# Performance work log

Hardware: AMD Instinct MI355X
Metric: run time of the kernel (lower is better)

## Reference

```python
import jax, jax.numpy as jnp
import numpy as np

B, S, D, H, E, K = 4, 2048, 1024, 512, 64, 8


def setup_inputs() -> dict:
    key = jax.random.key(0)
    k1, k2, k3, k4 = jax.random.split(key, 4)
    x = jax.random.normal(k1, (B, S, D), dtype=jnp.float32)
    # gate weight stored as [D, E] (equivalent to torch Linear weight [E, D] transposed)
    Wg = jax.random.normal(k2, (D, E), dtype=jnp.float32) * (1.0 / np.sqrt(D))
    Wup = jax.random.normal(k3, (E, D, H), dtype=jnp.float32) * (1.0 / np.sqrt(D))
    Wdown = jax.random.normal(k4, (E, H, D), dtype=jnp.float32) * (1.0 / np.sqrt(H))
    return {"x": x, "Wg": Wg, "Wup": Wup, "Wdown": Wdown}


def reference(x, Wg, Wup, Wdown):
    # NOTE: ExpertMLP.forward in the source ignores gate_proj: out = down(silu(up(x)))
    T = B * S
    flat = x.reshape(T, D)                        # [T, D]
    logits = flat @ Wg                            # [T, E]
    topk_scores, topk_idx = jax.lax.top_k(logits, K)   # [T, K]
    gate_w = jax.nn.softmax(topk_scores, axis=-1)       # [T, K]
    # dense combine matrix [T, E]; topk indices are unique per token
    rows = jnp.arange(T)[:, None]
    combine = jnp.zeros((T, E), dtype=x.dtype).at[rows, topk_idx].set(gate_w)
    # scan over experts: each expert runs on all tokens, masked/weighted by combine
    def body(acc, params):
        wu, wd, c = params                         # [D,H], [H,D], [T]
        h = jax.nn.silu(flat @ wu)                 # [T, H]
        y = h @ wd                                 # [T, D]
        return acc + c[:, None] * y, None
    out0 = jnp.zeros((T, D), dtype=x.dtype)
    out, _ = jax.lax.scan(body, out0, (Wup, Wdown, combine.T))
    return out.reshape(B, S, D)
```

## Files before the change

kernel.cpp:

```cpp
#include <hip/hip_runtime.h>
#include <hip/hip_bf16.h>
#include <stdint.h>
#include <math.h>

#define T_TOK 8192
#define DDIM  1024
#define HDIM  512
#define NEXP  64
#define TOPK  8
#define CHUNKS 16

typedef __bf16 bf16x8 __attribute__((ext_vector_type(8)));
typedef float  f32x4  __attribute__((ext_vector_type(4)));

__device__ __forceinline__ void load_lds16(const void* gp, void* lp){
  __builtin_amdgcn_global_load_lds(
      (__attribute__((address_space(1))) void*)(uintptr_t)gp,
      (__attribute__((address_space(3))) void*)lp, 16, 0, 0);
}

__device__ __forceinline__ unsigned short f2bfbits(float f){
  union { __bf16 b; unsigned short u; } cv; cv.b = (__bf16)f; return cv.u;
}
__device__ __forceinline__ float bf2f(unsigned short s){
  unsigned int u = ((unsigned int)s) << 16; return __uint_as_float(u);
}

__global__ __launch_bounds__(256) void k_cvt_x(const float* __restrict__ x,
                                               __bf16* __restrict__ xb){
  size_t i   = (size_t)blockIdx.x * 256 + threadIdx.x;
  size_t off = i * 8;
  float4 v0 = *(const float4*)(x + off);
  float4 v1 = *(const float4*)(x + off + 4);
  bf16x8 o;
  o[0]=(__bf16)v0.x; o[1]=(__bf16)v0.y; o[2]=(__bf16)v0.z; o[3]=(__bf16)v0.w;
  o[4]=(__bf16)v1.x; o[5]=(__bf16)v1.y; o[6]=(__bf16)v1.z; o[7]=(__bf16)v1.w;
  *(bf16x8*)(xb + off) = o;
}

__global__ __launch_bounds__(256) void k_transpose_cvt(const float* __restrict__ src,
                                                       __bf16* __restrict__ dst,
                                                       int R, int C){
  __shared__ float tile[32][33];
  int z  = blockIdx.z;
  int c0 = blockIdx.x * 32;
  int r0 = blockIdx.y * 32;
  const float* s = src + (size_t)z * R * C;
  __bf16*      d = dst + (size_t)z * R * C;
  int tx = threadIdx.x, ty = threadIdx.y;
  #pragma unroll
  for (int i = ty; i < 32; i += 8)
    tile[i][tx] = s[(size_t)(r0 + i) * C + c0 + tx];
  __syncthreads();
  #pragma unroll
  for (int i = ty; i < 32; i += 8)
    d[(size_t)(c0 + i) * R + r0 + tx] = (__bf16)tile[tx][i];
}

__global__ __launch_bounds__(256) void k_gate(const float* __restrict__ x,
                                              const float* __restrict__ Wg,
                                              float* __restrict__ logits){
  __shared__ float xs[32][64];
  __shared__ float ws[32][64];
  const int tid = threadIdx.x;
  const int m0  = blockIdx.x * 64;
  const int tm  = (tid >> 4) << 2;
  const int tn  = (tid & 15) << 2;
  const int sr  = tid >> 2;
  const int sc  = tid & 3;
  double acc[4][4];
  #pragma unroll
  for (int i=0;i<4;i++)
    #pragma unroll
    for (int j=0;j<4;j++) acc[i][j]=0.0;

  for (int k0 = 0; k0 < DDIM; k0 += 32){
    {
      const float4* g = (const float4*)(Wg + (size_t)k0 * 64);
      float4* l = (float4*)&ws[0][0];
      l[tid]       = g[tid];
      l[tid + 256] = g[tid + 256];
    }
    {
      const float* g = x + (size_t)(m0 + sr) * DDIM + k0 + sc * 8;
      float4 a = *(const float4*)g;
      float4 b = *(const float4*)(g + 4);
      xs[sc*8+0][sr]=a.x; xs[sc*8+1][sr]=a.y; xs[sc*8+2][sr]=a.z; xs[sc*8+3][sr]=a.w;
      xs[sc*8+4][sr]=b.x; xs[sc*8+5][sr]=b.y; xs[sc*8+6][sr]=b.z; xs[sc*8+7][sr]=b.w;
    }
    __syncthreads();
    for (int k = 0; k < 32; k++){
      float4 a4 = *(const float4*)&xs[k][tm];
      float4 b4 = *(const float4*)&ws[k][tn];
      float av[4] = {a4.x,a4.y,a4.z,a4.w};
      float bv[4] = {b4.x,b4.y,b4.z,b4.w};
      #pragma unroll
      for (int i=0;i<4;i++)
        #pragma unroll
        for (int j=0;j<4;j++)
          acc[i][j] += (double)av[i] * (double)bv[j];
    }
    __syncthreads();
  }
  #pragma unroll
  for (int i=0;i<4;i++){
    float4 o = make_float4((float)acc[i][0],(float)acc[i][1],(float)acc[i][2],(float)acc[i][3]);
    *(float4*)&logits[(size_t)(m0 + tm + i) * 64 + tn] = o;
  }
}

__global__ __launch_bounds__(256) void k_topk(const float* __restrict__ logits,
                                              int* __restrict__ tk_idx,
                                              float* __restrict__ tk_w){
  const int lane = threadIdx.x & 63;
  const int t    = blockIdx.x * 4 + (threadIdx.x >> 6);
  float v = logits[(size_t)t * 64 + lane];
  const int myi = lane;
  float mv[8]; int mi[8];
  #pragma unroll
  for (int k = 0; k < 8; k++){
    float bv = v; int bi = myi;
    #pragma unroll
    for (int off = 32; off > 0; off >>= 1){
      float ov = __shfl_xor(bv, off, 64);
      int   oi = __shfl_xor(bi, off, 64);
      if (ov > bv || (ov == bv && oi < bi)){ bv = ov; bi = oi; }
    }
    mv[k] = bv; mi[k] = bi;
    if (bi == myi) v = -INFINITY;
  }
  float w[8]; float s = 0.f;
  #pragma unroll
  for (int k = 0; k < 8; k++){ w[k] = expf(mv[k] - mv[0]); s += w[k]; }
  float inv = 1.0f / s;
  if (lane == 0){
    #pragma unroll
    for (int k = 0; k < 8; k++){
      tk_idx[(size_t)t * 8 + k] = mi[k];
      tk_w [(size_t)t * 8 + k] = w[k] * inv;
    }
  }
}

__global__ __launch_bounds__(256) void k_hist(const int* __restrict__ tk_idx,
                                              int* __restrict__ g_hist){
  __shared__ int h[4][64];
  const int tid = threadIdx.x, wave = tid >> 6;
  ((int*)h)[tid] = 0;
  __syncthreads();
  const int4* p = (const int4*)(tk_idx + blockIdx.x * 4096);
  #pragma unroll
  for (int i = 0; i < 4; i++){
    int4 v = p[i * 256 + tid];
    atomicAdd(&h[wave][v.x], 1); atomicAdd(&h[wave][v.y], 1);
    atomicAdd(&h[wave][v.z], 1); atomicAdd(&h[wave][v.w], 1);
  }
  __syncthreads();
  if (tid < 64)
    g_hist[blockIdx.x * 64 + tid] = h[0][tid] + h[1][tid] + h[2][tid] + h[3][tid];
}

__global__ void k_scan(const int* __restrict__ g_hist,
                       int* __restrict__ offsets,
                       int* __restrict__ g_base){
  const int e = threadIdx.x;
  int h[CHUNKS]; int tot = 0;
  #pragma unroll
  for (int c = 0; c < CHUNKS; c++){ h[c] = g_hist[c * 64 + e]; tot += h[c]; }
  int inc = tot;
  #pragma unroll
  for (int off = 1; off < 64; off <<= 1){
    int n = __shfl_up(inc, off, 64);
    if (e >= off) inc += n;
  }
  int exc = inc - tot;
  offsets[e] = exc;
  if (e == 63) offsets[64] = inc;
  int b = exc;
  #pragma unroll
  for (int c = 0; c < CHUNKS; c++){ g_base[c * 64 + e] = b; b += h[c]; }
}

__global__ __launch_bounds__(256) void k_scatter(const int* __restrict__ tk_idx,
                                                 const int* __restrict__ g_base,
                                                 int* __restrict__ slot_token,
                                                 int* __restrict__ inv_pos){
  __shared__ int cnt[64];
  const int tid = threadIdx.x;
  if (tid < 64) cnt[tid] = g_base[blockIdx.x * 64 + tid];
  __syncthreads();
  const int base = blockIdx.x * 4096;
  #pragma unroll
  for (int i = 0; i < 16; i++){
    int gid = base + i * 256 + tid;
    int e = tk_idx[gid];
    int pos = atomicAdd(&cnt[e], 1);
    slot_token[pos] = gid >> 3;
    inv_pos[gid] = pos;
  }
}

__global__ __launch_bounds__(256) void k_gemm1(const __bf16* __restrict__ xb,
                                               const __bf16* __restrict__ wupT,
                                               const int* __restrict__ offsets,
                                               const int* __restrict__ slot_token,
                                               __bf16* __restrict__ h){
  const int e    = blockIdx.z;
  const int base = offsets[e];
  const int ne   = offsets[e + 1] - base;
  const int m0   = blockIdx.x * 128;
  if (m0 >= ne) return;
  const int n0   = blockIdx.y * 128;

  __shared__ __align__(16) __bf16 As[128 * 32];
  __shared__ __align__(16) __bf16 Bs[128 * 32];
  __shared__ int s_tok[128];

  const int tid = threadIdx.x;
  if (tid < 128){
    int r = m0 + tid;
    s_tok[tid] = slot_token[base + (r < ne ? r : 0)];
  }
  __syncthreads();

  const int wave = tid >> 6, lane = tid & 63;
  const int wm = (wave >> 1) << 6, wn = (wave & 1) << 6;
  const int sr = lane >> 2, sc = lane & 3;
  const int fr = lane & 15, fk = (lane >> 4) << 3;
  const __bf16* wB = wupT + (size_t)e * HDIM * DDIM + (size_t)n0 * DDIM;

  f32x4 zero = {0.f, 0.f, 0.f, 0.f};
  f32x4 acc[4][4];
  #pragma unroll
  for (int i=0;i<4;i++)
    #pragma unroll
    for (int j=0;j<4;j++) acc[i][j] = zero;

  for (int k0 = 0; k0 < DDIM; k0 += 32){
    #pragma unroll
    for (int q = 0; q < 2; q++){
      int rr = (wave << 5) + (q << 4) + sr;
      const __bf16* g = xb + (size_t)s_tok[rr] * DDIM + k0 + (sc << 3);
      load_lds16(g, (void*)&As[((wave << 1) + q) << 9]);
    }
    #pragma unroll
    for (int q = 0; q < 2; q++){
      int rr = (wave << 5) + (q << 4) + sr;
      const __bf16* g = wB + (size_t)rr * DDIM + k0 + (sc << 3);
      load_lds16(g, (void*)&Bs[((wave << 1) + q) << 9]);
    }
    __syncthreads();
    bf16x8 af[4], bg[4];
    #pragma unroll
    for (int i=0;i<4;i++) af[i] = *(const bf16x8*)&As[((wm + (i<<4) + fr) << 5) + fk];
    #pragma unroll
    for (int j=0;j<4;j++) bg[j] = *(const bf16x8*)&Bs[((wn + (j<<4) + fr) << 5) + fk];
    #pragma unroll
    for (int i=0;i<4;i++)
      #pragma unroll
      for (int j=0;j<4;j++)
        acc[i][j] = __builtin_amdgcn_mfma_f32_16x16x32_bf16(af[i], bg[j], acc[i][j], 0, 0, 0);
    __syncthreads();
  }

  const int cr = (lane >> 4) << 2, cc = lane & 15;
  #pragma unroll
  for (int i=0;i<4;i++){
    #pragma unroll
    for (int reg=0;reg<4;reg++){
      int rl = wm + (i << 4) + cr + reg;
      int gm = m0 + rl;
      if (gm < ne){
        __bf16* hrow = h + (size_t)(base + gm) * HDIM + n0 + wn;
        #pragma unroll
        for (int j=0;j<4;j++){
          float v  = acc[i][j][reg];
          float sv = v / (1.0f + __expf(-v));
          unsigned short u = f2bfbits(sv);
          int part = __shfl_xor((int)u, 1, 64);
          if (!(lane & 1)){
            unsigned int packed = ((unsigned int)(unsigned short)part << 16) | u;
            *(unsigned int*)((unsigned short*)hrow + (j << 4) + cc) = packed;
          }
        }
      }
    }
  }
}

__global__ __launch_bounds__(256) void k_gemm2(const __bf16* __restrict__ h,
                                               const __bf16* __restrict__ wdownT,
                                               const int* __restrict__ offsets,
                                               __bf16* __restrict__ y,
                                               int elo){
  const int e    = elo + blockIdx.z;
  const int base = offsets[e];
  const int ne   = offsets[e + 1] - base;
  const int m0   = blockIdx.x * 128;
  if (m0 >= ne) return;
  const int n0   = blockIdx.y * 128;
  const int ybase = offsets[elo];

  __shared__ __align__(16) __bf16 As[128 * 32];
  __shared__ __align__(16) __bf16 Bs[128 * 32];

  const int tid = threadIdx.x;
  const int wave = tid >> 6, lane = tid & 63;
  const int wm = (wave >> 1) << 6, wn = (wave & 1) << 6;
  const int sr = lane >> 2, sc = lane & 3;
  const int fr = lane & 15, fk = (lane >> 4) << 3;
  const __bf16* wB = wdownT + (size_t)e * DDIM * HDIM + (size_t)n0 * HDIM;

  f32x4 zero = {0.f, 0.f, 0.f, 0.f};
  f32x4 acc[4][4];
  #pragma unroll
  for (int i=0;i<4;i++)
    #pragma unroll
    for (int j=0;j<4;j++) acc[i][j] = zero;

  for (int k0 = 0; k0 < HDIM; k0 += 32){
    #pragma unroll
    for (int q = 0; q < 2; q++){
      int rr = (wave << 5) + (q << 4) + sr;
      int sl = (m0 + rr < ne) ? (m0 + rr) : 0;
      const __bf16* g = h + (size_t)(base + sl) * HDIM + k0 + (sc << 3);
      load_lds16(g, (void*)&As[((wave << 1) + q) << 9]);
    }
    #pragma unroll
    for (int q = 0; q < 2; q++){
      int rr = (wave << 5) + (q << 4) + sr;
      const __bf16* g = wB + (size_t)rr * HDIM + k0 + (sc << 3);
      load_lds16(g, (void*)&Bs[((wave << 1) + q) << 9]);
    }
    __syncthreads();
    bf16x8 af[4], bg[4];
    #pragma unroll
    for (int i=0;i<4;i++) af[i] = *(const bf16x8*)&As[((wm + (i<<4) + fr) << 5) + fk];
    #pragma unroll
    for (int j=0;j<4;j++) bg[j] = *(const bf16x8*)&Bs[((wn + (j<<4) + fr) << 5) + fk];
    #pragma unroll
    for (int i=0;i<4;i++)
      #pragma unroll
      for (int j=0;j<4;j++)
        acc[i][j] = __builtin_amdgcn_mfma_f32_16x16x32_bf16(af[i], bg[j], acc[i][j], 0, 0, 0);
    __syncthreads();
  }

  const int cr = (lane >> 4) << 2, cc = lane & 15;
  #pragma unroll
  for (int i=0;i<4;i++){
    #pragma unroll
    for (int reg=0;reg<4;reg++){
      int rl = wm + (i << 4) + cr + reg;
      int gm = m0 + rl;
      if (gm < ne){
        __bf16* yrow = y + (size_t)(base - ybase + gm) * DDIM + n0 + wn;
        #pragma unroll
        for (int j=0;j<4;j++){
          unsigned short u = f2bfbits(acc[i][j][reg]);
          int part = __shfl_xor((int)u, 1, 64);
          if (!(lane & 1)){
            unsigned int packed = ((unsigned int)(unsigned short)part << 16) | u;
            *(unsigned int*)((unsigned short*)yrow + (j << 4) + cc) = packed;
          }
        }
      }
    }
  }
}

__global__ __launch_bounds__(256) void k_combine(const __bf16* __restrict__ y,
                                                 const int* __restrict__ tk_idx,
                                                 const float* __restrict__ tk_w,
                                                 const int* __restrict__ inv_pos,
                                                 const int* __restrict__ offsets,
                                                 float* __restrict__ out,
                                                 int elo, int ehi, int first){
  const int t   = blockIdx.x;
  const int tid = threadIdx.x;
  __shared__ int se[8]; __shared__ float sw[8]; __shared__ int sp[8];
  if (tid < 8){
    se[tid] = tk_idx[(size_t)t * 8 + tid];
    sw[tid] = tk_w [(size_t)t * 8 + tid];
    sp[tid] = inv_pos[(size_t)t * 8 + tid];
  }
  __syncthreads();
  const int ybase = offsets[elo];
  const int c = tid << 2;
  float4 acc;
  if (first) acc = make_float4(0.f, 0.f, 0.f, 0.f);
  else       acc = *(const float4*)&out[(size_t)t * DDIM + c];
  #pragma unroll
  for (int k = 0; k < 8; k++){
    int e = se[k];
    if (e >= elo && e < ehi){
      const unsigned short* yr = (const unsigned short*)y + (size_t)(sp[k] - ybase) * DDIM + c;
      ushort4 raw = *(const ushort4*)yr;
      float w = sw[k];
      acc.x += w * bf2f(raw.x);
      acc.y += w * bf2f(raw.y);
      acc.z += w * bf2f(raw.z);
      acc.w += w * bf2f(raw.w);
    }
  }
  *(float4*)&out[(size_t)t * DDIM + c] = acc;
}

extern "C" void kernel_launch(void* const* d_in, const int* in_sizes, int n_in,
                              void* d_out, int out_size, void* d_ws, size_t ws_size,
                              hipStream_t stream){
  const float* x     = (const float*)d_in[0];
  const float* Wg    = (const float*)d_in[1];
  const float* Wup   = (const float*)d_in[2];
  const float* Wdown = (const float*)d_in[3];
  float* out = (float*)d_out;

  char* ws = (char*)d_ws;
  size_t off = 0;
  auto alloc = [&](size_t bytes) -> void* {
    void* p = ws + off;
    off += (bytes + 255) & ~(size_t)255;
    return p;
  };
  __bf16* wupT      = (__bf16*)alloc((size_t)NEXP * DDIM * HDIM * 2);
  __bf16* xb        = (__bf16*)alloc((size_t)T_TOK * DDIM * 2);
  float*  logits    = (float*)alloc((size_t)T_TOK * NEXP * 4);
  __bf16* wdownT    = (__bf16*)alloc((size_t)NEXP * DDIM * HDIM * 2);
  __bf16* hbuf      = (__bf16*)alloc((size_t)T_TOK * TOPK * HDIM * 2);
  int*    tk_idx    = (int*)  alloc((size_t)T_TOK * TOPK * 4);
  float*  tk_w      = (float*)alloc((size_t)T_TOK * TOPK * 4);
  int*    slot_tok  = (int*)  alloc((size_t)T_TOK * TOPK * 4);
  int*    inv_pos   = (int*)  alloc((size_t)T_TOK * TOPK * 4);
  int*    g_hist    = (int*)  alloc((size_t)CHUNKS * 64 * 4);
  int*    g_base    = (int*)  alloc((size_t)CHUNKS * 64 * 4);
  int*    offsets   = (int*)  alloc(512);
  __bf16* ybuf      = (__bf16*)ws;

  k_cvt_x<<<4096, 256, 0, stream>>>(x, xb);
  k_transpose_cvt<<<dim3(16, 32, 64), dim3(32, 8), 0, stream>>>(Wup,   wupT,   DDIM, HDIM);
  k_transpose_cvt<<<dim3(32, 16, 64), dim3(32, 8), 0, stream>>>(Wdown, wdownT, HDIM, DDIM);
  k_gate<<<T_TOK / 64, 256, 0, stream>>>(x, Wg, logits);
  k_topk<<<T_TOK / 4, 256, 0, stream>>>(logits, tk_idx, tk_w);
  k_hist<<<CHUNKS, 256, 0, stream>>>(tk_idx, g_hist);
  k_scan<<<1, 64, 0, stream>>>(g_hist, offsets, g_base);
  k_scatter<<<CHUNKS, 256, 0, stream>>>(tk_idx, g_base, slot_tok, inv_pos);
  k_gemm1<<<dim3(16, 4, 64), 256, 0, stream>>>(xb, wupT, offsets, slot_tok, hbuf);
  k_gemm2<<<dim3(16, 8, 32), 256, 0, stream>>>(hbuf, wdownT, offsets, ybuf, 0);
  k_combine<<<T_TOK, 256, 0, stream>>>(ybuf, tk_idx, tk_w, inv_pos, offsets, out, 0, 32, 1);
  k_gemm2<<<dim3(16, 8, 32), 256, 0, stream>>>(hbuf, wdownT, offsets, ybuf, 32);
  k_combine<<<T_TOK, 256, 0, stream>>>(ybuf, tk_idx, tk_w, inv_pos, offsets, out, 32, 64, 0);
}
```

Baseline: 705.1 us.

## Double-buffer LDS tiles in both expert GEMM kernels to overlap loads with MFMA

Both grouped GEMM kernels now use two LDS buffers for A and B tiles. The next K-slice is prefetched with global_load_lds while MFMAs run on the current one, replacing the load-sync-compute-sync sequence. Per-thread global pointers are also hoisted out of the K loop. This doubles LDS use per block, which may lower occupancy. Correctness depends on the loop-end barrier, which is not shown, to order buffer reuse.

New measurement: 756.1 us. 7.2% more time.

```diff
diff --git a/kernel.cpp b/kernel.cpp
--- a/kernel.cpp
+++ b/kernel.cpp
@@ -212,8 +212,8 @@
   if (m0 >= ne) return;
   const int n0   = blockIdx.y * 128;
 
-  __shared__ __align__(16) __bf16 As[128 * 32];
-  __shared__ __align__(16) __bf16 Bs[128 * 32];
+  __shared__ __align__(16) __bf16 As[2][128 * 32];
+  __shared__ __align__(16) __bf16 Bs[2][128 * 32];
   __shared__ int s_tok[128];
 
   const int tid = threadIdx.x;
@@ -229,6 +229,13 @@
   const int fr = lane & 15, fk = (lane >> 4) << 3;
   const __bf16* wB = wupT + (size_t)e * HDIM * DDIM + (size_t)n0 * DDIM;
 
+  const int rr0 = (wave << 5) + sr, rr1 = rr0 + 16;
+  const __bf16* gA0 = xb + (size_t)s_tok[rr0] * DDIM + (sc << 3);
+  const __bf16* gA1 = xb + (size_t)s_tok[rr1] * DDIM + (sc << 3);
+  const __bf16* gB0 = wB + (size_t)rr0 * DDIM + (sc << 3);
+  const __bf16* gB1 = wB + (size_t)rr1 * DDIM + (sc << 3);
+  const int ld0 = (wave << 1) << 9, ld1 = ((wave << 1) + 1) << 9;
+
   f32x4 zero = {0.f, 0.f, 0.f, 0.f};
   f32x4 acc[4][4];
   #pragma unroll
@@ -236,25 +243,28 @@
     #pragma unroll
     for (int j=0;j<4;j++) acc[i][j] = zero;
 
-  for (int k0 = 0; k0 < DDIM; k0 += 32){
-    #pragma unroll
-    for (int q = 0; q < 2; q++){
-      int rr = (wave << 5) + (q << 4) + sr;
-      const __bf16* g = xb + (size_t)s_tok[rr] * DDIM + k0 + (sc << 3);
-      load_lds16(g, (void*)&As[((wave << 1) + q) << 9]);
-    }
-    #pragma unroll
-    for (int q = 0; q < 2; q++){
-      int rr = (wave << 5) + (q << 4) + sr;
-      const __bf16* g = wB + (size_t)rr * DDIM + k0 + (sc << 3);
-      load_lds16(g, (void*)&Bs[((wave << 1) + q) << 9]);
-    }
-    __syncthreads();
+  load_lds16(gA0, (void*)&As[0][ld0]);
+  load_lds16(gA1, (void*)&As[0][ld1]);
+  load_lds16(gB0, (void*)&Bs[0][ld0]);
+  load_lds16(gB1, (void*)&Bs[0][ld1]);
+  __syncthreads();
+
+  const int NK = DDIM / 32;
+  for (int t = 0; t < NK; ++t){
+    const int cur = t & 1;
+    if (t + 1 < NK){
+      const int k1 = (t + 1) << 5;
+      const int nxt = cur ^ 1;
+      load_lds16(gA0 + k1, (void*)&As[nxt][ld0]);
+      load_lds16(gA1 + k1, (void*)&As[nxt][ld1]);
+      load_lds16(gB0 + k1, (void*)&Bs[nxt][ld0]);
+      load_lds16(gB1 + k1, (void*)&Bs[nxt][ld1]);
+    }
     bf16x8 af[4], bg[4];
     #pragma unroll
-    for (int i=0;i<4;i++) af[i] = *(const bf16x8*)&As[((wm + (i<<4) + fr) << 5) + fk];
-    #pragma unroll
-    for (int j=0;j<4;j++) bg[j] = *(const bf16x8*)&Bs[((wn + (j<<4) + fr) << 5) + fk];
+    for (int i=0;i<4;i++) af[i] = *(const bf16x8*)&As[cur][((wm + (i<<4) + fr) << 5) + fk];
+    #pragma unroll
+    for (int j=0;j<4;j++) bg[j] = *(const bf16x8*)&Bs[cur][((wn + (j<<4) + fr) << 5) + fk];
     #pragma unroll
     for (int i=0;i<4;i++)
       #pragma unroll
@@ -301,8 +311,8 @@
   const int n0   = blockIdx.y * 128;
   const int ybase = offsets[elo];
 
-  __shared__ __align__(16) __bf16 As[128 * 32];
-  __shared__ __align__(16) __bf16 Bs[128 * 32];
+  __shared__ __align__(16) __bf16 As[2][128 * 32];
+  __shared__ __align__(16) __bf16 Bs[2][128 * 32];
 
   const int tid = threadIdx.x;
   const int wave = tid >> 6, lane = tid & 63;
@@ -311,6 +321,15 @@
   const int fr = lane & 15, fk = (lane >> 4) << 3;
   const __bf16* wB = wdownT + (size_t)e * DDIM * HDIM + (size_t)n0 * HDIM;
 
+  const int rr0 = (wave << 5) + sr, rr1 = rr0 + 16;
+  const int sl0 = (m0 + rr0 < ne) ? (m0 + rr0) : 0;
+  const int sl1 = (m0 + rr1 < ne) ? (m0 + rr1) : 0;
+  const __bf16* gA0 = h + (size_t)(base + sl0) * HDIM + (sc << 3);
+  const __bf16* gA1 = h + (size_t)(base + sl1) * HDIM + (sc << 3);
+  const __bf16* gB0 = wB + (size_t)rr0 * HDIM + (sc << 3);
+  const __bf16* gB1 = wB + (size_t)rr1 * HDIM + (sc << 3);
+  const int ld0 = (wave << 1) << 9, ld1 = ((wave << 1) + 1) << 9;
+
   f32x4 zero = {0.f, 0.f, 0.f, 0.f};
   f32x4 acc[4][4];
   #pragma unroll
@@ -318,26 +337,28 @@
     #pragma unroll
     for (int j=0;j<4;j++) acc[i][j] = zero;
 
-  for (int k0 = 0; k0 < HDIM; k0 += 32){
-    #pragma unroll
-    for (int q = 0; q < 2; q++){
-      int rr = (wave << 5) + (q << 4) + sr;
-      int sl = (m0 + rr < ne) ? (m0 + rr) : 0;
-      const __bf16* g = h + (size_t)(base + sl) * HDIM + k0 + (sc << 3);
-      load_lds16(g, (void*)&As[((wave << 1) + q) << 9]);
-    }
-    #pragma unroll
-    for (int q = 0; q < 2; q++){
-      int rr = (wave << 5) + (q << 4) + sr;
-      const __bf16* g = wB + (size_t)rr * HDIM + k0 + (sc << 3);
-      load_lds16(g, (void*)&Bs[((wave << 1) + q) << 9]);
-    }
-    __syncthreads();
+  load_lds16(gA0, (void*)&As[0][ld0]);
+  load_lds16(gA1, (void*)&As[0][ld1]);
+  load_lds16(gB0, (void*)&Bs[0][ld0]);
+  load_lds16(gB1, (void*)&Bs[0][ld1]);
+  __syncthreads();
+
+  const int NK = HDIM / 32;
+  for (int t = 0; t < NK; ++t){
+    const int cur = t & 1;
+    if (t + 1 < NK){
+      const int k1 = (t + 1) << 5;
+      const int nxt = cur ^ 1;
+      load_lds16(gA0 + k1, (void*)&As[nxt][ld0]);
+      load_lds16(gA1 + k1, (void*)&As[nxt][ld1]);
+      load_lds16(gB0 + k1, (void*)&Bs[nxt][ld0]);
+      load_lds16(gB1 + k1, (void*)&Bs[nxt][ld1]);
+    }
     bf16x8 af[4], bg[4];
     #pragma unroll
-    for (int i=0;i<4;i++) af[i] = *(const bf16x8*)&As[((wm + (i<<4) + fr) << 5) + fk];
-    #pragma unroll
-    for (int j=0;j<4;j++) bg[j] = *(const bf16x8*)&Bs[((wn + (j<<4) + fr) << 5) + fk];
+    for (int i=0;i<4;i++) af[i] = *(const bf16x8*)&As[cur][((wm + (i<<4) + fr) << 5) + fk];
+    #pragma unroll
+    for (int j=0;j<4;j++) bg[j] = *(const bf16x8*)&Bs[cur][((wn + (j<<4) + fr) << 5) + fk];
     #pragma unroll
     for (int i=0;i<4;i++)
       #pragma unroll
```

## Enlarge grouped GEMM tiles to 256x256x64 with double-buffered LDS and 512 threads

Applied to the files above, without the earlier changes.

Both expert GEMMs now use 256x256 output tiles with 64-wide K steps, 8 waves per block, and double-buffered LDS. The next K-tile is prefetched via global_load_lds while the current one is consumed by MFMA. This aims to improve operand reuse per byte loaded, halve barrier count, and overlap loads with compute. It costs 128KB of LDS per block, which allows only one block per CU, plus 128 accumulator registers per lane and coarser padding waste for experts with few tokens.

Result: slower. 733.1 us (+4.0%).

```diff
diff --git a/kernel.cpp b/kernel.cpp
--- a/kernel.cpp
+++ b/kernel.cpp
@@ -200,7 +200,8 @@
   }
 }
 
-__global__ __launch_bounds__(256) void k_gemm1(const __bf16* __restrict__ xb,
+
+__global__ __launch_bounds__(512) void k_gemm1(const __bf16* __restrict__ xb,
                                                const __bf16* __restrict__ wupT,
                                                const int* __restrict__ offsets,
                                                const int* __restrict__ slot_token,
@@ -208,64 +209,82 @@
   const int e    = blockIdx.z;
   const int base = offsets[e];
   const int ne   = offsets[e + 1] - base;
-  const int m0   = blockIdx.x * 128;
+  const int m0   = blockIdx.x * 256;
   if (m0 >= ne) return;
-  const int n0   = blockIdx.y * 128;
-
-  __shared__ __align__(16) __bf16 As[128 * 32];
-  __shared__ __align__(16) __bf16 Bs[128 * 32];
-  __shared__ int s_tok[128];
+  const int n0   = blockIdx.y * 256;
+
+  __shared__ __align__(16) __bf16 As[2][256 * 64];
+  __shared__ __align__(16) __bf16 Bs[2][256 * 64];
+  __shared__ int s_tok[256];
 
   const int tid = threadIdx.x;
-  if (tid < 128){
+  if (tid < 256){
     int r = m0 + tid;
-    s_tok[tid] = slot_token[base + (r < ne ? r : 0)];
+    s_tok[tid] = slot_token[base + (r < ne ? r : (ne - 1))];
   }
   __syncthreads();
 
   const int wave = tid >> 6, lane = tid & 63;
-  const int wm = (wave >> 1) << 6, wn = (wave & 1) << 6;
-  const int sr = lane >> 2, sc = lane & 3;
+  const int wm = (wave >> 2) << 7;
+  const int wn = (wave & 3) << 6;
   const int fr = lane & 15, fk = (lane >> 4) << 3;
   const __bf16* wB = wupT + (size_t)e * HDIM * DDIM + (size_t)n0 * DDIM;
 
-  f32x4 zero = {0.f, 0.f, 0.f, 0.f};
-  f32x4 acc[4][4];
-  #pragma unroll
-  for (int i=0;i<4;i++)
-    #pragma unroll
-    for (int j=0;j<4;j++) acc[i][j] = zero;
-
-  for (int k0 = 0; k0 < DDIM; k0 += 32){
-    #pragma unroll
-    for (int q = 0; q < 2; q++){
-      int rr = (wave << 5) + (q << 4) + sr;
-      const __bf16* g = xb + (size_t)s_tok[rr] * DDIM + k0 + (sc << 3);
-      load_lds16(g, (void*)&As[((wave << 1) + q) << 9]);
-    }
-    #pragma unroll
-    for (int q = 0; q < 2; q++){
-      int rr = (wave << 5) + (q << 4) + sr;
-      const __bf16* g = wB + (size_t)rr * DDIM + k0 + (sc << 3);
-      load_lds16(g, (void*)&Bs[((wave << 1) + q) << 9]);
+  const int srow = (wave << 3) + (lane >> 3);
+  const int scol = (lane & 7) << 3;
+  const __bf16* gA[4]; const __bf16* gB[4]; int ldsOff[4];
+  #pragma unroll
+  for (int q = 0; q < 4; q++){
+    int r = (q << 6) + srow;
+    gA[q] = xb + (size_t)s_tok[r] * DDIM + scol;
+    gB[q] = wB + (size_t)(r) * DDIM + scol;
+    ldsOff[q] = (q << 12) + (wave << 9);
+  }
+
+  f32x4 acc[8][4];
+  #pragma unroll
+  for (int i=0;i<8;i++)
+    #pragma unroll
+    for (int j=0;j<4;j++) acc[i][j] = (f32x4){0.f,0.f,0.f,0.f};
+
+  #pragma unroll
+  for (int q = 0; q < 4; q++){
+    load_lds16(gA[q], (void*)&As[0][ldsOff[q]]);
+    load_lds16(gB[q], (void*)&Bs[0][ldsOff[q]]);
+  }
+  __syncthreads();
+
+  const int NK = DDIM / 64;
+  for (int t = 0; t < NK; ++t){
+    const int cur = t & 1;
+    if (t + 1 < NK){
+      const int k1 = (t + 1) << 6;
+      const int nxt = cur ^ 1;
+      #pragma unroll
+      for (int q = 0; q < 4; q++){
+        load_lds16(gA[q] + k1, (void*)&As[nxt][ldsOff[q]]);
+        load_lds16(gB[q] + k1, (void*)&Bs[nxt][ldsOff[q]]);
+      }
+    }
+    #pragma unroll
+    for (int ks = 0; ks < 2; ks++){
+      bf16x8 af[8], bg[4];
+      #pragma unroll
+      for (int i=0;i<8;i++) af[i] = *(const bf16x8*)&As[cur][((wm + (i<<4) + fr) << 6) + (ks<<5) + fk];
+      #pragma unroll
+      for (int j=0;j<4;j++) bg[j] = *(const bf16x8*)&Bs[cur][((wn + (j<<4) + fr) << 6) + (ks<<5) + fk];
+      #pragma unroll
+      for (int i=0;i<8;i++)
+        #pragma unroll
+        for (int j=0;j<4;j++)
+          acc[i][j] = __builtin_amdgcn_mfma_f32_16x16x32_bf16(af[i], bg[j], acc[i][j], 0, 0, 0);
     }
     __syncthreads();
-    bf16x8 af[4], bg[4];
-    #pragma unroll
-    for (int i=0;i<4;i++) af[i] = *(const bf16x8*)&As[((wm + (i<<4) + fr) << 5) + fk];
-    #pragma unroll
-    for (int j=0;j<4;j++) bg[j] = *(const bf16x8*)&Bs[((wn + (j<<4) + fr) << 5) + fk];
-    #pragma unroll
-    for (int i=0;i<4;i++)
-      #pragma unroll
-      for (int j=0;j<4;j++)
-        acc[i][j] = __builtin_amdgcn_mfma_f32_16x16x32_bf16(af[i], bg[j], acc[i][j], 0, 0, 0);
-    __syncthreads();
   }
 
   const int cr = (lane >> 4) << 2, cc = lane & 15;
   #pragma unroll
-  for (int i=0;i<4;i++){
+  for (int i=0;i<8;i++){
     #pragma unroll
     for (int reg=0;reg<4;reg++){
       int rl = wm + (i << 4) + cr + reg;
@@ -288,7 +307,7 @@
   }
 }
 
-__global__ __launch_bounds__(256) void k_gemm2(const __bf16* __restrict__ h,
+__global__ __launch_bounds__(512) void k_gemm2(const __bf16* __restrict__ h,
                                                const __bf16* __restrict__ wdownT,
                                                const int* __restrict__ offsets,
                                                __bf16* __restrict__ y,
@@ -296,59 +315,77 @@
   const int e    = elo + blockIdx.z;
   const int base = offsets[e];
   const int ne   = offsets[e + 1] - base;
-  const int m0   = blockIdx.x * 128;
+  const int m0   = blockIdx.x * 256;
   if (m0 >= ne) return;
-  const int n0   = blockIdx.y * 128;
+  const int n0   = blockIdx.y * 256;
   const int ybase = offsets[elo];
 
-  __shared__ __align__(16) __bf16 As[128 * 32];
-  __shared__ __align__(16) __bf16 Bs[128 * 32];
+  __shared__ __align__(16) __bf16 As[2][256 * 64];
+  __shared__ __align__(16) __bf16 Bs[2][256 * 64];
 
   const int tid = threadIdx.x;
   const int wave = tid >> 6, lane = tid & 63;
-  const int wm = (wave >> 1) << 6, wn = (wave & 1) << 6;
-  const int sr = lane >> 2, sc = lane & 3;
+  const int wm = (wave >> 2) << 7;
+  const int wn = (wave & 3) << 6;
   const int fr = lane & 15, fk = (lane >> 4) << 3;
   const __bf16* wB = wdownT + (size_t)e * DDIM * HDIM + (size_t)n0 * HDIM;
 
-  f32x4 zero = {0.f, 0.f, 0.f, 0.f};
-  f32x4 acc[4][4];
-  #pragma unroll
-  for (int i=0;i<4;i++)
-    #pragma unroll
-    for (int j=0;j<4;j++) acc[i][j] = zero;
-
-  for (int k0 = 0; k0 < HDIM; k0 += 32){
-    #pragma unroll
-    for (int q = 0; q < 2; q++){
-      int rr = (wave << 5) + (q << 4) + sr;
-      int sl = (m0 + rr < ne) ? (m0 + rr) : 0;
-      const __bf16* g = h + (size_t)(base + sl) * HDIM + k0 + (sc << 3);
-      load_lds16(g, (void*)&As[((wave << 1) + q) << 9]);
-    }
-    #pragma unroll
-    for (int q = 0; q < 2; q++){
-      int rr = (wave << 5) + (q << 4) + sr;
-      const __bf16* g = wB + (size_t)rr * HDIM + k0 + (sc << 3);
-      load_lds16(g, (void*)&Bs[((wave << 1) + q) << 9]);
+  const int srow = (wave << 3) + (lane >> 3);
+  const int scol = (lane & 7) << 3;
+  const __bf16* gA[4]; const __bf16* gB[4]; int ldsOff[4];
+  #pragma unroll
+  for (int q = 0; q < 4; q++){
+    int r = (q << 6) + srow;
+    int sl = m0 + r; if (sl >= ne) sl = ne - 1;
+    gA[q] = h + (size_t)(base + sl) * HDIM + scol;
+    gB[q] = wB + (size_t)r * HDIM + scol;
+    ldsOff[q] = (q << 12) + (wave << 9);
+  }
+
+  f32x4 acc[8][4];
+  #pragma unroll
+  for (int i=0;i<8;i++)
+    #pragma unroll
+    for (int j=0;j<4;j++) acc[i][j] = (f32x4){0.f,0.f,0.f,0.f};
+
+  #pragma unroll
+  for (int q = 0; q < 4; q++){
+    load_lds16(gA[q], (void*)&As[0][ldsOff[q]]);
+    load_lds16(gB[q], (void*)&Bs[0][ldsOff[q]]);
+  }
+  __syncthreads();
+
+  const int NK = HDIM / 64;
+  for (int t = 0; t < NK; ++t){
+    const int cur = t & 1;
+    if (t + 1 < NK){
+      const int k1 = (t + 1) << 6;
+      const int nxt = cur ^ 1;
+      #pragma unroll
+      for (int q = 0; q < 4; q++){
+        load_lds16(gA[q] + k1, (void*)&As[nxt][ldsOff[q]]);
+        load_lds16(gB[q] + k1, (void*)&Bs[nxt][ldsOff[q]]);
+      }
+    }
+    #pragma unroll
+    for (int ks = 0; ks < 2; ks++){
+      bf16x8 af[8], bg[4];
+      #pragma unroll
+      for (int i=0;i<8;i++) af[i] = *(const bf16x8*)&As[cur][((wm + (i<<4) + fr) << 6) + (ks<<5) + fk];
+      #pragma unroll
+      for (int j=0;j<4;j++) bg[j] = *(const bf16x8*)&Bs[cur][((wn + (j<<4) + fr) << 6) + (ks<<5) + fk];
+      #pragma unroll
+      for (int i=0;i<8;i++)
+        #pragma unroll
+        for (int j=0;j<4;j++)
+          acc[i][j] = __builtin_amdgcn_mfma_f32_16x16x32_bf16(af[i], bg[j], acc[i][j], 0, 0, 0);
     }
     __syncthreads();
-    bf16x8 af[4], bg[4];
-    #pragma unroll
-    for (int i=0;i<4;i++) af[i] = *(const bf16x8*)&As[((wm + (i<<4) + fr) << 5) + fk];
-    #pragma unroll
-    for (int j=0;j<4;j++) bg[j] = *(const bf16x8*)&Bs[((wn + (j<<4) + fr) << 5) + fk];
-    #pragma unroll
-    for (int i=0;i<4;i++)
-      #pragma unroll
-      for (int j=0;j<4;j++)
-        acc[i][j] = __builtin_amdgcn_mfma_f32_16x16x32_bf16(af[i], bg[j], acc[i][j], 0, 0, 0);
-    __syncthreads();
   }
 
   const int cr = (lane >> 4) << 2, cc = lane & 15;
   #pragma unroll
-  for (int i=0;i<4;i++){
+  for (int i=0;i<8;i++){
     #pragma unroll
     for (int reg=0;reg<4;reg++){
       int rl = wm + (i << 4) + cr + reg;
@@ -444,9 +481,9 @@
   k_hist<<<CHUNKS, 256, 0, stream>>>(tk_idx, g_hist);
   k_scan<<<1, 64, 0, stream>>>(g_hist, offsets, g_base);
   k_scatter<<<CHUNKS, 256, 0, stream>>>(tk_idx, g_base, slot_tok, inv_pos);
-  k_gemm1<<<dim3(16, 4, 64), 256, 0, stream>>>(xb, wupT, offsets, slot_tok, hbuf);
-  k_gemm2<<<dim3(16, 8, 32), 256, 0, stream>>>(hbuf, wdownT, offsets, ybuf, 0);
+  k_gemm1<<<dim3(8, 2, 64), 512, 0, stream>>>(xb, wupT, offsets, slot_tok, hbuf);
+  k_gemm2<<<dim3(8, 4, 32), 512, 0, stream>>>(hbuf, wdownT, offsets, ybuf, 0);
   k_combine<<<T_TOK, 256, 0, stream>>>(ybuf, tk_idx, tk_w, inv_pos, offsets, out, 0, 32, 1);
-  k_gemm2<<<dim3(16, 8, 32), 256, 0, stream>>>(hbuf, wdownT, offsets, ybuf, 32);
+  k_gemm2<<<dim3(8, 4, 32), 512, 0, stream>>>(hbuf, wdownT, offsets, ybuf, 32);
   k_combine<<<T_TOK, 256, 0, stream>>>(ybuf, tk_idx, tk_w, inv_pos, offsets, out, 32, 64, 0);
 }
```
